# Kernel tuning notes

Hardware: AMD Instinct MI355X
Metric: run time of the kernel (lower is better)

## Reference

```python
import jax, jax.numpy as jnp
import numpy as np

B, R, C, O, I = 128, 1152, 10, 16, 338  # batch, num_routes, num_capsules, out_channels, in_channels
NUM_ITER = 3


def setup_inputs() -> dict:
    key = jax.random.key(0)
    kx, kw = jax.random.split(key)
    x = jax.random.normal(kx, (B, R, I), dtype=jnp.float32)
    W = jax.random.normal(kw, (R, C, O, I), dtype=jnp.float32)  # leading batch-1 dim of torch param dropped
    return {"x": x, "W": W}


def _squash_elementwise(s):
    # torch squash over the trailing singleton dim of s_j (B,1,C,O,1):
    # squared_norm = s**2 elementwise -> out = s*|s|/(1+s**2)
    sq = s * s
    return sq * s / ((1.0 + sq) * jnp.sqrt(sq))


def reference(x, W):
    # u_hat[b,r,c,o] = sum_i W[r,c,o,i] * x[b,r,i]
    u_hat = jnp.einsum('rcoi,bri->brco', W, x)
    b_ij = jnp.zeros((R, C), dtype=x.dtype)  # logits shared across batch
    v = None
    for it in range(NUM_ITER):
        # F.softmax(b_ij) with no dim on 4D (1,R,C,1) defaults to dim=1 -> routes axis
        c_ij = jax.nn.softmax(b_ij, axis=0)  # (R, C)
        s = jnp.einsum('rc,brco->bco', c_ij, u_hat)  # (B, C, O)
        v = _squash_elementwise(s)
        if it < NUM_ITER - 1:
            # agreement: dot over O, then mean over batch
            a = jnp.einsum('brco,bco->brc', u_hat, v).mean(axis=0)  # (R, C)
            b_ij = b_ij + a
    # torch returns v_j.squeeze(1): (B, C, O, 1)
    return v[..., None]
```

## Files before the change

### kernel.cpp

```cpp
#include <hip/hip_runtime.h>
#include <math.h>

#define B_    128
#define R_    1152
#define C_    10
#define O_    16
#define I_    338
#define CO_   160
#define SLAB  20480
#define RS_CHUNKS 16
#define R_PER_CHUNK 72

#define KT32   32
#define NKT32  11
#define TAIL   18
#define LROW   40

typedef __attribute__((ext_vector_type(8))) short bf16x8;
typedef __attribute__((ext_vector_type(4))) float f32x4;

__device__ __forceinline__ unsigned short bf16_rne(float f) {
    unsigned int u = __float_as_uint(f);
    return (unsigned short)((u + 0x7fffu + ((u >> 16) & 1u)) >> 16);
}
__device__ __forceinline__ void cvt_split3(float f, unsigned short* h,
                                           unsigned short* m, unsigned short* l) {
    unsigned short hb = bf16_rne(f);
    float fh = __uint_as_float(((unsigned int)hb) << 16);
    float r1 = f - fh;
    unsigned short mb = bf16_rne(r1);
    float fm = __uint_as_float(((unsigned int)mb) << 16);
    float r2 = r1 - fm;
    unsigned short lb = bf16_rne(r2);
    *h = hb; *m = mb; *l = lb;
}

__global__ __launch_bounds__(256, 2) void uhat_kernel(const float* __restrict__ x,
                                                      const float* __restrict__ W,
                                                      float* __restrict__ u) {
    __shared__ __align__(16) unsigned short xh[128 * LROW];
    __shared__ __align__(16) unsigned short xm[128 * LROW];
    __shared__ __align__(16) unsigned short xl[128 * LROW];
    __shared__ __align__(16) unsigned short wh[160 * LROW];
    __shared__ __align__(16) unsigned short wm[160 * LROW];
    __shared__ __align__(16) unsigned short wl[160 * LROW];

    const int r    = blockIdx.x;
    const int tid  = threadIdx.x;
    const int lane = tid & 63;
    const int w    = tid >> 6;
    const int lr   = lane & 15;
    const int kq8  = (lane >> 4) * 8;

    f32x4 acc[2][10];
#pragma unroll
    for (int mt = 0; mt < 2; ++mt)
#pragma unroll
        for (int n = 0; n < 10; ++n) acc[mt][n] = (f32x4){0.f, 0.f, 0.f, 0.f};

    const float* xr = x + (size_t)r * I_;
    const float* wr = W + (size_t)r * (CO_ * I_);

    for (int kt = 0; kt < NKT32; ++kt) {
        const int k0 = kt * KT32;
        if (kt != NKT32 - 1) {
#pragma unroll
            for (int it = 0; it < 4; ++it) {
                int q = tid + it * 256;
                int b = q >> 3, kq = q & 7;
                const float* src = xr + (size_t)b * (R_ * I_) + k0 + kq * 4;
                float4 f = *(const float4*)src;
                ushort4 hv, mv, lv;
                cvt_split3(f.x, &hv.x, &mv.x, &lv.x);
                cvt_split3(f.y, &hv.y, &mv.y, &lv.y);
                cvt_split3(f.z, &hv.z, &mv.z, &lv.z);
                cvt_split3(f.w, &hv.w, &mv.w, &lv.w);
                *(ushort4*)&xh[b * LROW + kq * 4] = hv;
                *(ushort4*)&xm[b * LROW + kq * 4] = mv;
                *(ushort4*)&xl[b * LROW + kq * 4] = lv;
            }
#pragma unroll
            for (int it = 0; it < 5; ++it) {
                int q = tid + it * 256;
                int co = q >> 3, kq = q & 7;
                const float* src = wr + (size_t)co * I_ + k0 + kq * 4;
                float4 f = *(const float4*)src;
                ushort4 hv, mv, lv;
                cvt_split3(f.x, &hv.x, &mv.x, &lv.x);
                cvt_split3(f.y, &hv.y, &mv.y, &lv.y);
                cvt_split3(f.z, &hv.z, &mv.z, &lv.z);
                cvt_split3(f.w, &hv.w, &mv.w, &lv.w);
                *(ushort4*)&wh[co * LROW + kq * 4] = hv;
                *(ushort4*)&wm[co * LROW + kq * 4] = mv;
                *(ushort4*)&wl[co * LROW + kq * 4] = lv;
            }
        } else {
#pragma unroll
            for (int it = 0; it < 4; ++it) {
                int q = tid + it * 256;
                int b = q >> 3, kq = q & 7;
                const float* src = xr + (size_t)b * (R_ * I_) + k0;
                unsigned short hv[4], mv[4], lv[4];
#pragma unroll
                for (int j = 0; j < 4; ++j) {
                    int kk = kq * 4 + j;
                    float f = (kk < TAIL) ? src[kk] : 0.f;
                    cvt_split3(f, &hv[j], &mv[j], &lv[j]);
                }
                *(ushort4*)&xh[b * LROW + kq * 4] = make_ushort4(hv[0], hv[1], hv[2], hv[3]);
                *(ushort4*)&xm[b * LROW + kq * 4] = make_ushort4(mv[0], mv[1], mv[2], mv[3]);
                *(ushort4*)&xl[b * LROW + kq * 4] = make_ushort4(lv[0], lv[1], lv[2], lv[3]);
            }
#pragma unroll
            for (int it = 0; it < 5; ++it) {
                int q = tid + it * 256;
                int co = q >> 3, kq = q & 7;
                const float* src = wr + (size_t)co * I_ + k0;
                unsigned short hv[4], mv[4], lv[4];
#pragma unroll
                for (int j = 0; j < 4; ++j) {
                    int kk = kq * 4 + j;
                    float f = (kk < TAIL) ? src[kk] : 0.f;
                    cvt_split3(f, &hv[j], &mv[j], &lv[j]);
                }
                *(ushort4*)&wh[co * LROW + kq * 4] = make_ushort4(hv[0], hv[1], hv[2], hv[3]);
                *(ushort4*)&wm[co * LROW + kq * 4] = make_ushort4(mv[0], mv[1], mv[2], mv[3]);
                *(ushort4*)&wl[co * LROW + kq * 4] = make_ushort4(lv[0], lv[1], lv[2], lv[3]);
            }
        }
        __syncthreads();

        bf16x8 ah[2], am[2], al[2];
#pragma unroll
        for (int mt = 0; mt < 2; ++mt) {
            int row = w * 32 + mt * 16 + lr;
            ah[mt] = *(const bf16x8*)&xh[row * LROW + kq8];
            am[mt] = *(const bf16x8*)&xm[row * LROW + kq8];
            al[mt] = *(const bf16x8*)&xl[row * LROW + kq8];
        }
#pragma unroll
        for (int n = 0; n < 10; ++n) {
            int co = n * 16 + lr;
            bf16x8 bh = *(const bf16x8*)&wh[co * LROW + kq8];
            bf16x8 bm = *(const bf16x8*)&wm[co * LROW + kq8];
            bf16x8 bl = *(const bf16x8*)&wl[co * LROW + kq8];
#pragma unroll
            for (int mt = 0; mt < 2; ++mt) {
                acc[mt][n] = __builtin_amdgcn_mfma_f32_16x16x32_bf16(ah[mt], bh, acc[mt][n], 0, 0, 0);
                acc[mt][n] = __builtin_amdgcn_mfma_f32_16x16x32_bf16(ah[mt], bm, acc[mt][n], 0, 0, 0);
                acc[mt][n] = __builtin_amdgcn_mfma_f32_16x16x32_bf16(am[mt], bh, acc[mt][n], 0, 0, 0);
                acc[mt][n] = __builtin_amdgcn_mfma_f32_16x16x32_bf16(ah[mt], bl, acc[mt][n], 0, 0, 0);
                acc[mt][n] = __builtin_amdgcn_mfma_f32_16x16x32_bf16(am[mt], bm, acc[mt][n], 0, 0, 0);
                acc[mt][n] = __builtin_amdgcn_mfma_f32_16x16x32_bf16(al[mt], bh, acc[mt][n], 0, 0, 0);
            }
        }
        __syncthreads();
    }

    float* ur = u + (size_t)r * SLAB;
    const int rquad = (lane >> 4) * 4;
#pragma unroll
    for (int mt = 0; mt < 2; ++mt)
#pragma unroll
        for (int n = 0; n < 10; ++n)
#pragma unroll
            for (int reg = 0; reg < 4; ++reg) {
                int b = w * 32 + mt * 16 + rquad + reg;
                ur[b * CO_ + n * 16 + lr] = acc[mt][n][reg];
            }
}

__global__ void softmax_kernel(const float* __restrict__ bij, float* __restrict__ cij) {
    const int c   = blockIdx.x;
    const int tid = threadIdx.x;
    __shared__ float redm[4];
    __shared__ float reds[4];
    __shared__ float bcast[2];

    float m = -1e30f;
    for (int r = tid; r < R_; r += 256) m = fmaxf(m, bij[r * C_ + c]);
#pragma unroll
    for (int off = 32; off > 0; off >>= 1) m = fmaxf(m, __shfl_down(m, off));
    if ((tid & 63) == 0) redm[tid >> 6] = m;
    __syncthreads();
    if (tid == 0) bcast[0] = fmaxf(fmaxf(redm[0], redm[1]), fmaxf(redm[2], redm[3]));
    __syncthreads();
    m = bcast[0];

    float s = 0.f;
    for (int r = tid; r < R_; r += 256) s += expf(bij[r * C_ + c] - m);
#pragma unroll
    for (int off = 32; off > 0; off >>= 1) s += __shfl_down(s, off);
    if ((tid & 63) == 0) reds[tid >> 6] = s;
    __syncthreads();
    if (tid == 0) bcast[1] = reds[0] + reds[1] + reds[2] + reds[3];
    __syncthreads();
    const float inv = 1.0f / bcast[1];
    for (int r = tid; r < R_; r += 256) cij[r * C_ + c] = expf(bij[r * C_ + c] - m) * inv;
}

__global__ void v_partial_kernel(const float* __restrict__ u, const float* __restrict__ cij,
                                 float* __restrict__ partial) {
    const int idx   = blockIdx.x * 256 + threadIdx.x;
    const int chunk = blockIdx.y;
    const int c     = (idx >> 4) % 10;
    const int r0    = chunk * R_PER_CHUNK;
    const float* up = u + (size_t)r0 * SLAB + idx;
    const float* cp = cij + r0 * C_ + c;
    float s = 0.f;
#pragma unroll 4
    for (int rr = 0; rr < R_PER_CHUNK; ++rr)
        s = fmaf(cp[rr * C_], up[(size_t)rr * SLAB], s);
    partial[chunk * SLAB + idx] = s;
}

__global__ void v_finalize_kernel(const float* __restrict__ partial, float* __restrict__ v) {
    const int idx = blockIdx.x * 256 + threadIdx.x;
    float s = 0.f;
#pragma unroll
    for (int ch = 0; ch < RS_CHUNKS; ++ch) s += partial[ch * SLAB + idx];
    v[idx] = s * fabsf(s) / (1.0f + s * s);
}

__global__ void agree_kernel(const float* __restrict__ u, const float* __restrict__ v,
                             float* __restrict__ bij) {
    const int r = blockIdx.x;
    const int l = threadIdx.x;
    const int c = threadIdx.y;
    const float* ur = u + (size_t)r * SLAB;
    float acc = 0.f;
#pragma unroll 4
    for (int k = l; k < B_ * O_; k += 64) {
        int b = k >> 4, o = k & 15;
        int off = b * CO_ + c * O_ + o;
        acc = fmaf(ur[off], v[off], acc);
    }
#pragma unroll
    for (int off = 32; off > 0; off >>= 1) acc += __shfl_down(acc, off);
    if (l == 0) bij[r * C_ + c] += acc * (1.0f / B_);
}

extern "C" void kernel_launch(void* const* d_in, const int* in_sizes, int n_in,
                              void* d_out, int out_size, void* d_ws, size_t ws_size,
                              hipStream_t stream) {
    const float* x = (const float*)d_in[0];
    const float* W = (const float*)d_in[1];
    float* out = (float*)d_out;

    float* ws      = (float*)d_ws;
    float* u       = ws;
    float* bij     = u + (size_t)R_ * SLAB;
    float* cij     = bij + R_ * C_;
    float* partial = cij + R_ * C_;
    float* v       = partial + RS_CHUNKS * SLAB;

    hipMemsetAsync(bij, 0, R_ * C_ * sizeof(float), stream);
    uhat_kernel<<<R_, 256, 0, stream>>>(x, W, u);

    for (int it = 0; it < 3; ++it) {
        softmax_kernel<<<C_, 256, 0, stream>>>(bij, cij);
        dim3 g(SLAB / 256, RS_CHUNKS);
        v_partial_kernel<<<g, 256, 0, stream>>>(u, cij, partial);
        float* vout = (it == 2) ? out : v;
        v_finalize_kernel<<<SLAB / 256, 256, 0, stream>>>(partial, vout);
        if (it < 2) agree_kernel<<<R_, dim3(64, 10), 0, stream>>>(u, v, bij);
    }
}
```

Baseline: 637.4 us.

## Double-buffer uhat LDS tiles with swizzle and vectorize routing kernels with float4

```diff
diff --git a/kernel.cpp b/kernel.cpp
--- a/kernel.cpp
+++ b/kernel.cpp
@@ -14,7 +14,14 @@
 #define KT32   32
 #define NKT32  11
 #define TAIL   18
-#define LROW   40
+#define LROWU  32
+#define RXH    0
+#define RXM    128
+#define RXL    256
+#define RWH    384
+#define RWM    544
+#define RWL    704
+#define BUFU   (864 * LROWU)
 
 typedef __attribute__((ext_vector_type(8))) short bf16x8;
 typedef __attribute__((ext_vector_type(4))) float f32x4;
@@ -35,115 +42,125 @@
     *h = hb; *m = mb; *l = lb;
 }
 
-__global__ __launch_bounds__(256, 2) void uhat_kernel(const float* __restrict__ x,
-                                                      const float* __restrict__ W,
-                                                      float* __restrict__ u) {
-    __shared__ __align__(16) unsigned short xh[128 * LROW];
-    __shared__ __align__(16) unsigned short xm[128 * LROW];
-    __shared__ __align__(16) unsigned short xl[128 * LROW];
-    __shared__ __align__(16) unsigned short wh[160 * LROW];
-    __shared__ __align__(16) unsigned short wm[160 * LROW];
-    __shared__ __align__(16) unsigned short wl[160 * LROW];
+__global__ __launch_bounds__(256) void uhat_kernel(const float* __restrict__ x,
+                                                   const float* __restrict__ W,
+                                                   float* __restrict__ u) {
+    __shared__ __align__(16) unsigned short lds[2][BUFU];
 
     const int r    = blockIdx.x;
     const int tid  = threadIdx.x;
     const int lane = tid & 63;
     const int w    = tid >> 6;
     const int lr   = lane & 15;
-    const int kq8  = (lane >> 4) * 8;
-
-    f32x4 acc[2][10];
-#pragma unroll
-    for (int mt = 0; mt < 2; ++mt)
-#pragma unroll
-        for (int n = 0; n < 10; ++n) acc[mt][n] = (f32x4){0.f, 0.f, 0.f, 0.f};
+    const int hi   = lane >> 4;
+    const int cSw  = (hi + lr + (lr >> 2)) & 3;
+
+    const int r0s = tid >> 3;
+    const int kqx = tid & 7;
+    const int cWw = ((kqx >> 1) + r0s + (r0s >> 2)) & 3;
+    const int eo  = (kqx & 1) * 4;
 
     const float* xr = x + (size_t)r * I_;
     const float* wr = W + (size_t)r * (CO_ * I_);
 
-    for (int kt = 0; kt < NKT32; ++kt) {
+    float4 fx[4], fw[5];
+
+    auto issue_loads = [&](int kt) {
         const int k0 = kt * KT32;
         if (kt != NKT32 - 1) {
 #pragma unroll
             for (int it = 0; it < 4; ++it) {
-                int q = tid + it * 256;
-                int b = q >> 3, kq = q & 7;
-                const float* src = xr + (size_t)b * (R_ * I_) + k0 + kq * 4;
-                float4 f = *(const float4*)src;
-                ushort4 hv, mv, lv;
-                cvt_split3(f.x, &hv.x, &mv.x, &lv.x);
-                cvt_split3(f.y, &hv.y, &mv.y, &lv.y);
-                cvt_split3(f.z, &hv.z, &mv.z, &lv.z);
-                cvt_split3(f.w, &hv.w, &mv.w, &lv.w);
-                *(ushort4*)&xh[b * LROW + kq * 4] = hv;
-                *(ushort4*)&xm[b * LROW + kq * 4] = mv;
-                *(ushort4*)&xl[b * LROW + kq * 4] = lv;
+                int b = r0s + it * 32;
+                fx[it] = *(const float4*)(xr + (size_t)b * (R_ * I_) + k0 + kqx * 4);
             }
 #pragma unroll
             for (int it = 0; it < 5; ++it) {
-                int q = tid + it * 256;
-                int co = q >> 3, kq = q & 7;
-                const float* src = wr + (size_t)co * I_ + k0 + kq * 4;
-                float4 f = *(const float4*)src;
-                ushort4 hv, mv, lv;
-                cvt_split3(f.x, &hv.x, &mv.x, &lv.x);
-                cvt_split3(f.y, &hv.y, &mv.y, &lv.y);
-                cvt_split3(f.z, &hv.z, &mv.z, &lv.z);
-                cvt_split3(f.w, &hv.w, &mv.w, &lv.w);
-                *(ushort4*)&wh[co * LROW + kq * 4] = hv;
-                *(ushort4*)&wm[co * LROW + kq * 4] = mv;
-                *(ushort4*)&wl[co * LROW + kq * 4] = lv;
+                int co = r0s + it * 32;
+                fw[it] = *(const float4*)(wr + (size_t)co * I_ + k0 + kqx * 4);
             }
         } else {
+            const int kb = kqx * 4;
 #pragma unroll
             for (int it = 0; it < 4; ++it) {
-                int q = tid + it * 256;
-                int b = q >> 3, kq = q & 7;
-                const float* src = xr + (size_t)b * (R_ * I_) + k0;
-                unsigned short hv[4], mv[4], lv[4];
-#pragma unroll
-                for (int j = 0; j < 4; ++j) {
-                    int kk = kq * 4 + j;
-                    float f = (kk < TAIL) ? src[kk] : 0.f;
-                    cvt_split3(f, &hv[j], &mv[j], &lv[j]);
-                }
-                *(ushort4*)&xh[b * LROW + kq * 4] = make_ushort4(hv[0], hv[1], hv[2], hv[3]);
-                *(ushort4*)&xm[b * LROW + kq * 4] = make_ushort4(mv[0], mv[1], mv[2], mv[3]);
-                *(ushort4*)&xl[b * LROW + kq * 4] = make_ushort4(lv[0], lv[1], lv[2], lv[3]);
+                int b = r0s + it * 32;
+                const float* s = xr + (size_t)b * (R_ * I_) + k0 + kb;
+                float4 f;
+                f.x = (kb + 0 < TAIL) ? s[0] : 0.f;
+                f.y = (kb + 1 < TAIL) ? s[1] : 0.f;
+                f.z = (kb + 2 < TAIL) ? s[2] : 0.f;
+                f.w = (kb + 3 < TAIL) ? s[3] : 0.f;
+                fx[it] = f;
             }
 #pragma unroll
             for (int it = 0; it < 5; ++it) {
-                int q = tid + it * 256;
-                int co = q >> 3, kq = q & 7;
-                const float* src = wr + (size_t)co * I_ + k0;
-                unsigned short hv[4], mv[4], lv[4];
-#pragma unroll
-                for (int j = 0; j < 4; ++j) {
-                    int kk = kq * 4 + j;
-                    float f = (kk < TAIL) ? src[kk] : 0.f;
-                    cvt_split3(f, &hv[j], &mv[j], &lv[j]);
-                }
-                *(ushort4*)&wh[co * LROW + kq * 4] = make_ushort4(hv[0], hv[1], hv[2], hv[3]);
-                *(ushort4*)&wm[co * LROW + kq * 4] = make_ushort4(mv[0], mv[1], mv[2], mv[3]);
-                *(ushort4*)&wl[co * LROW + kq * 4] = make_ushort4(lv[0], lv[1], lv[2], lv[3]);
-            }
-        }
-        __syncthreads();
-
+                int co = r0s + it * 32;
+                const float* s = wr + (size_t)co * I_ + k0 + kb;
+                float4 f;
+                f.x = (kb + 0 < TAIL) ? s[0] : 0.f;
+                f.y = (kb + 1 < TAIL) ? s[1] : 0.f;
+                f.z = (kb + 2 < TAIL) ? s[2] : 0.f;
+                f.w = (kb + 3 < TAIL) ? s[3] : 0.f;
+                fw[it] = f;
+            }
+        }
+    };
+
+    auto cvt_store = [&](int buf) {
+        unsigned short* L = &lds[buf][0];
+#pragma unroll
+        for (int it = 0; it < 4; ++it) {
+            int row = r0s + it * 32;
+            float4 f = fx[it];
+            ushort4 hv, mv, lv;
+            cvt_split3(f.x, &hv.x, &mv.x, &lv.x);
+            cvt_split3(f.y, &hv.y, &mv.y, &lv.y);
+            cvt_split3(f.z, &hv.z, &mv.z, &lv.z);
+            cvt_split3(f.w, &hv.w, &mv.w, &lv.w);
+            int off = (RXH + row) * LROWU + cWw * 8 + eo;
+            *(ushort4*)&L[off]                         = hv;
+            *(ushort4*)&L[off + (RXM - RXH) * LROWU]   = mv;
+            *(ushort4*)&L[off + (RXL - RXH) * LROWU]   = lv;
+        }
+#pragma unroll
+        for (int it = 0; it < 5; ++it) {
+            int row = r0s + it * 32;
+            float4 f = fw[it];
+            ushort4 hv, mv, lv;
+            cvt_split3(f.x, &hv.x, &mv.x, &lv.x);
+            cvt_split3(f.y, &hv.y, &mv.y, &lv.y);
+            cvt_split3(f.z, &hv.z, &mv.z, &lv.z);
+            cvt_split3(f.w, &hv.w, &mv.w, &lv.w);
+            int off = (RWH + row) * LROWU + cWw * 8 + eo;
+            *(ushort4*)&L[off]                         = hv;
+            *(ushort4*)&L[off + (RWM - RWH) * LROWU]   = mv;
+            *(ushort4*)&L[off + (RWL - RWH) * LROWU]   = lv;
+        }
+    };
+
+    f32x4 acc[2][10];
+#pragma unroll
+    for (int mt = 0; mt < 2; ++mt)
+#pragma unroll
+        for (int n = 0; n < 10; ++n) acc[mt][n] = (f32x4){0.f, 0.f, 0.f, 0.f};
+
+    auto compute = [&](int buf) {
+        const unsigned short* L = &lds[buf][0];
         bf16x8 ah[2], am[2], al[2];
 #pragma unroll
         for (int mt = 0; mt < 2; ++mt) {
             int row = w * 32 + mt * 16 + lr;
-            ah[mt] = *(const bf16x8*)&xh[row * LROW + kq8];
-            am[mt] = *(const bf16x8*)&xm[row * LROW + kq8];
-            al[mt] = *(const bf16x8*)&xl[row * LROW + kq8];
+            int off = (RXH + row) * LROWU + cSw * 8;
+            ah[mt] = *(const bf16x8*)&L[off];
+            am[mt] = *(const bf16x8*)&L[off + (RXM - RXH) * LROWU];
+            al[mt] = *(const bf16x8*)&L[off + (RXL - RXH) * LROWU];
         }
 #pragma unroll
         for (int n = 0; n < 10; ++n) {
             int co = n * 16 + lr;
-            bf16x8 bh = *(const bf16x8*)&wh[co * LROW + kq8];
-            bf16x8 bm = *(const bf16x8*)&wm[co * LROW + kq8];
-            bf16x8 bl = *(const bf16x8*)&wl[co * LROW + kq8];
+            int off = (RWH + co) * LROWU + cSw * 8;
+            bf16x8 bh = *(const bf16x8*)&L[off];
+            bf16x8 bm = *(const bf16x8*)&L[off + (RWM - RWH) * LROWU];
+            bf16x8 bl = *(const bf16x8*)&L[off + (RWL - RWH) * LROWU];
 #pragma unroll
             for (int mt = 0; mt < 2; ++mt) {
                 acc[mt][n] = __builtin_amdgcn_mfma_f32_16x16x32_bf16(ah[mt], bh, acc[mt][n], 0, 0, 0);
@@ -154,11 +171,20 @@
                 acc[mt][n] = __builtin_amdgcn_mfma_f32_16x16x32_bf16(al[mt], bh, acc[mt][n], 0, 0, 0);
             }
         }
+    };
+
+    issue_loads(0);
+    cvt_store(0);
+    __syncthreads();
+    for (int t = 0; t < NKT32; ++t) {
+        if (t + 1 < NKT32) issue_loads(t + 1);
+        compute(t & 1);
+        if (t + 1 < NKT32) cvt_store((t + 1) & 1);
         __syncthreads();
     }
 
     float* ur = u + (size_t)r * SLAB;
-    const int rquad = (lane >> 4) * 4;
+    const int rquad = hi * 4;
 #pragma unroll
     for (int mt = 0; mt < 2; ++mt)
 #pragma unroll
@@ -201,25 +227,41 @@
 
 __global__ void v_partial_kernel(const float* __restrict__ u, const float* __restrict__ cij,
                                  float* __restrict__ partial) {
-    const int idx   = blockIdx.x * 256 + threadIdx.x;
+    const int q     = blockIdx.x * 256 + threadIdx.x;
+    const int idx   = q << 2;
     const int chunk = blockIdx.y;
     const int c     = (idx >> 4) % 10;
     const int r0    = chunk * R_PER_CHUNK;
-    const float* up = u + (size_t)r0 * SLAB + idx;
-    const float* cp = cij + r0 * C_ + c;
-    float s = 0.f;
-#pragma unroll 4
-    for (int rr = 0; rr < R_PER_CHUNK; ++rr)
-        s = fmaf(cp[rr * C_], up[(size_t)rr * SLAB], s);
-    partial[chunk * SLAB + idx] = s;
+    const float4* up = (const float4*)(u + (size_t)r0 * SLAB + idx);
+    const float* cp  = cij + r0 * C_ + c;
+    float4 s = {0.f, 0.f, 0.f, 0.f};
+#pragma unroll 8
+    for (int rr = 0; rr < R_PER_CHUNK; ++rr) {
+        float  cv = cp[rr * C_];
+        float4 uu = up[(size_t)rr * (SLAB / 4)];
+        s.x = fmaf(cv, uu.x, s.x);
+        s.y = fmaf(cv, uu.y, s.y);
+        s.z = fmaf(cv, uu.z, s.z);
+        s.w = fmaf(cv, uu.w, s.w);
+    }
+    *(float4*)(partial + (size_t)chunk * SLAB + idx) = s;
 }
 
 __global__ void v_finalize_kernel(const float* __restrict__ partial, float* __restrict__ v) {
-    const int idx = blockIdx.x * 256 + threadIdx.x;
-    float s = 0.f;
-#pragma unroll
-    for (int ch = 0; ch < RS_CHUNKS; ++ch) s += partial[ch * SLAB + idx];
-    v[idx] = s * fabsf(s) / (1.0f + s * s);
+    const int q   = blockIdx.x * 256 + threadIdx.x;
+    const int idx = q << 2;
+    float4 s = {0.f, 0.f, 0.f, 0.f};
+#pragma unroll
+    for (int ch = 0; ch < RS_CHUNKS; ++ch) {
+        float4 p = *(const float4*)(partial + (size_t)ch * SLAB + idx);
+        s.x += p.x; s.y += p.y; s.z += p.z; s.w += p.w;
+    }
+    float4 o;
+    o.x = s.x * fabsf(s.x) / (1.0f + s.x * s.x);
+    o.y = s.y * fabsf(s.y) / (1.0f + s.y * s.y);
+    o.z = s.z * fabsf(s.z) / (1.0f + s.z * s.z);
+    o.w = s.w * fabsf(s.w) / (1.0f + s.w * s.w);
+    *(float4*)(v + idx) = o;
 }
 
 __global__ void agree_kernel(const float* __restrict__ u, const float* __restrict__ v,
@@ -230,10 +272,15 @@
     const float* ur = u + (size_t)r * SLAB;
     float acc = 0.f;
 #pragma unroll 4
-    for (int k = l; k < B_ * O_; k += 64) {
-        int b = k >> 4, o = k & 15;
-        int off = b * CO_ + c * O_ + o;
-        acc = fmaf(ur[off], v[off], acc);
+    for (int k = l; k < B_ * 4; k += 64) {
+        int b = k >> 2, oq = k & 3;
+        int off = b * CO_ + c * O_ + oq * 4;
+        float4 uu = *(const float4*)&ur[off];
+        float4 vv = *(const float4*)&v[off];
+        acc = fmaf(uu.x, vv.x, acc);
+        acc = fmaf(uu.y, vv.y, acc);
+        acc = fmaf(uu.z, vv.z, acc);
+        acc = fmaf(uu.w, vv.w, acc);
     }
 #pragma unroll
     for (int off = 32; off > 0; off >>= 1) acc += __shfl_down(acc, off);
@@ -259,10 +306,10 @@
 
     for (int it = 0; it < 3; ++it) {
         softmax_kernel<<<C_, 256, 0, stream>>>(bij, cij);
-        dim3 g(SLAB / 256, RS_CHUNKS);
+        dim3 g(SLAB / 1024, RS_CHUNKS);
         v_partial_kernel<<<g, 256, 0, stream>>>(u, cij, partial);
         float* vout = (it == 2) ? out : v;
-        v_finalize_kernel<<<SLAB / 256, 256, 0, stream>>>(partial, vout);
+        v_finalize_kernel<<<SLAB / 1024, 256, 0, stream>>>(partial, vout);
         if (it < 2) agree_kernel<<<R_, dim3(64, 10), 0, stream>>>(u, v, bij);
     }
 }
```

Measured after the change: 674.4 us. +5.8%, slower.
